# Kernel optimization log

Hardware: AMD Instinct MI355X
Metric: run time of the kernel (lower is better)

Reference implementation:

```python
import jax, jax.numpy as jnp
import numpy as np

NEG_SLOPE = 0.2
N_NODES, N_EDGES, N_FEAT, N_GRAPHS = 50000, 400000, 128, 64


def _glorot(k, shape):
    return jax.random.normal(k, shape, jnp.float32) / jnp.sqrt(jnp.float32(shape[0]))


def setup_inputs() -> dict:
    key = jax.random.key(0)
    ks = jax.random.split(key, 12)
    return {
        "x": jax.random.normal(ks[0], (N_NODES, N_FEAT), jnp.float32),
        "edge_index": jax.random.randint(ks[1], (2, N_EDGES), 0, N_NODES),
        "batch": jnp.sort(jax.random.randint(ks[2], (N_NODES,), 0, N_GRAPHS)),
        "W1": _glorot(ks[3], (N_FEAT, 64)),
        "as1": jax.random.normal(ks[4], (4, 16), jnp.float32) * 0.1,
        "ad1": jax.random.normal(ks[5], (4, 16), jnp.float32) * 0.1,
        "b1": jnp.zeros((64,), jnp.float32),
        "W2": _glorot(ks[6], (64, 256)),
        "as2": jax.random.normal(ks[7], (4, 64), jnp.float32) * 0.1,
        "ad2": jax.random.normal(ks[8], (4, 64), jnp.float32) * 0.1,
        "b2": jnp.zeros((256,), jnp.float32),
        "W3": _glorot(ks[9], (256, 512)),
        "as3": jax.random.normal(ks[10], (4, 128), jnp.float32) * 0.1,
        "ad3": jax.random.normal(ks[11], (4, 128), jnp.float32) * 0.1,
        "b3": jnp.zeros((128,), jnp.float32),
        "Wlin": _glorot(jax.random.fold_in(key, 99), (128, 10)),
        "blin": jnp.zeros((10,), jnp.float32),
    }


def _gat(x, src, dst, W, a_src, a_dst, b, concat, n):
    # PyG GATConv: per-head linear, LeakyReLU edge scores, segment softmax over
    # incoming edges of dst, weighted scatter-aggregate, then bias.
    H, C = a_src.shape
    h = (x @ W).reshape(n, H, C)                       # [N,H,C]
    es = jnp.einsum('nhc,hc->nh', h, a_src)            # score contrib of source node
    ed = jnp.einsum('nhc,hc->nh', h, a_dst)            # score contrib of target node
    e = jax.nn.leaky_relu(es[src] + ed[dst], NEG_SLOPE)  # [E,H]
    m = jax.ops.segment_max(e, dst, num_segments=n)
    m = jnp.where(jnp.isfinite(m), m, jnp.float32(0.0))
    ex = jnp.exp(e - m[dst])
    den = jax.ops.segment_sum(ex, dst, num_segments=n)
    alpha = ex / (den[dst] + jnp.float32(1e-16))       # [E,H]
    out = jax.ops.segment_sum(alpha[:, :, None] * h[src], dst, num_segments=n)  # [N,H,C]
    out = out.reshape(n, H * C) if concat else out.mean(axis=1)
    return out + b


def reference(x, edge_index, batch, W1, as1, ad1, b1, W2, as2, ad2, b2,
              W3, as3, ad3, b3, Wlin, blin):
    n = x.shape[0]
    loop = jnp.arange(n)
    src = jnp.concatenate([edge_index[0], loop])  # add self-loops (PyG default)
    dst = jnp.concatenate([edge_index[1], loop])
    h = jax.nn.elu(_gat(x, src, dst, W1, as1, ad1, b1, True, n))
    h = jax.nn.elu(_gat(h, src, dst, W2, as2, ad2, b2, True, n))
    h = jax.nn.elu(_gat(h, src, dst, W3, as3, ad3, b3, False, n))
    # global mean pool over graphs
    s = jax.ops.segment_sum(h, batch, num_segments=N_GRAPHS)
    cnt = jax.ops.segment_sum(jnp.ones((n,), h.dtype), batch, num_segments=N_GRAPHS)
    pooled = s / jnp.maximum(cnt, jnp.float32(1.0))[:, None]
    # dropout is identity in eval mode
    return pooled @ Wlin + blin
```

## Files before the change

kernel.cpp:

```cpp
#include <hip/hip_runtime.h>
#include <math.h>

#define NNODES 50000
#define NEDGES 400000
#define ETOT   (NEDGES + NNODES)
#define NGRAPHS 64

typedef _Float16 f16;
typedef _Float16 f16x4 __attribute__((ext_vector_type(4)));
typedef _Float16 f16x8 __attribute__((ext_vector_type(8)));
typedef float f32x4 __attribute__((ext_vector_type(4)));

__device__ __forceinline__ float lrelu(float x){ return x >= 0.f ? x : 0.2f*x; }
__device__ __forceinline__ float eluf(float x){ return x > 0.f ? x : expm1f(x); }

__global__ void k_one(int* __restrict__ deg){
  int i = blockIdx.x*256 + threadIdx.x;
  if (i < NNODES) deg[i] = 1;
}
__global__ void k_hist(const int* __restrict__ ei, int* __restrict__ deg){
  int e = blockIdx.x*blockDim.x + threadIdx.x;
  if (e < NEDGES) atomicAdd(&deg[ei[NEDGES + e]], 1);
}
__global__ void k_scan1(const int* __restrict__ deg, int* __restrict__ part, int n){
  __shared__ int buf[256];
  int i = blockIdx.x*256 + threadIdx.x;
  buf[threadIdx.x] = (i<n)? deg[i] : 0;
  __syncthreads();
  for (int s=128; s>0; s>>=1){ if (threadIdx.x < s) buf[threadIdx.x]+=buf[threadIdx.x+s]; __syncthreads(); }
  if (threadIdx.x==0) part[blockIdx.x]=buf[0];
}
__global__ void k_scan2(const int* __restrict__ part, int* __restrict__ bpre, int* __restrict__ row_off_last, int nb){
  __shared__ int buf[256];
  int t = threadIdx.x;
  int v = (t<nb)? part[t] : 0;
  buf[t]=v; __syncthreads();
  for (int s=1;s<256;s<<=1){ int a = (t>=s)? buf[t-s]:0; __syncthreads(); buf[t]+=a; __syncthreads(); }
  if (t<nb) bpre[t] = buf[t]-v;
  if (t==255) row_off_last[0] = buf[255];
}
__global__ void k_scan3(const int* __restrict__ deg, const int* __restrict__ bpre, int* __restrict__ row_off, int n){
  __shared__ int buf[256];
  int t = threadIdx.x;
  int i = blockIdx.x*256 + t;
  int v = (i<n)? deg[i]:0;
  buf[t]=v; __syncthreads();
  for (int s=1;s<256;s<<=1){ int a=(t>=s)?buf[t-s]:0; __syncthreads(); buf[t]+=a; __syncthreads(); }
  if (i<n) row_off[i] = bpre[blockIdx.x] + buf[t]-v;
}
__global__ void k_selfpos(const int* __restrict__ row_off, int* __restrict__ csr_src,
                          int* __restrict__ csr_dst, int* __restrict__ cursor){
  int n = blockIdx.x*256 + threadIdx.x;
  if (n < NNODES){
    int p = row_off[n];
    csr_src[p] = n; csr_dst[p] = n;
    cursor[n] = 1;
  }
}
__global__ void k_scatter(const int* __restrict__ ei, const int* __restrict__ row_off,
                          int* __restrict__ cursor, int* __restrict__ csr_src, int* __restrict__ csr_dst){
  int e = blockIdx.x*blockDim.x + threadIdx.x;
  if (e < NEDGES){
    int s = ei[e], d = ei[NEDGES+e];
    int pos = row_off[d] + atomicAdd(&cursor[d],1);
    csr_src[pos] = s; csr_dst[pos] = d;
  }
}

__global__ void k_prep(const float* __restrict__ W1, const float* __restrict__ W2, const float* __restrict__ W3,
                       const float* __restrict__ as1, const float* __restrict__ ad1,
                       const float* __restrict__ as2, const float* __restrict__ ad2,
                       const float* __restrict__ as3, const float* __restrict__ ad3,
                       f16* __restrict__ BT1, f16* __restrict__ BT2, f16* __restrict__ BT3y,
                       f16* __restrict__ PT1, f16* __restrict__ PT2, f16* __restrict__ PT3){
  int u = blockIdx.x*256 + threadIdx.x;
  if (u < 8192){ int j=u>>7, k=u&127; BT1[j*128+k] = (f16)W1[(size_t)k*64+j]; return; }
  u -= 8192;
  if (u < 16384){ int col=u>>6, k=u&63; BT2[col*64+k] = (f16)W2[(size_t)k*256+col]; return; }
  u -= 16384;
  if (u < 131072){ int j=u>>8, k=u&255;
                   BT3y[(size_t)j*256+k] = (f16)W3[(size_t)k*512 + j]; return; }
  u -= 131072;
  if (u < 1024){
    int o=u>>6, k=u&63; float v=0.f;
    if (o<8){ int h=o&3; if ((k>>4)==h) v = ((o<4)?as1:ad1)[h*16 + (k&15)]; }
    PT1[u] = (f16)v; return; }
  u -= 1024;
  if (u < 1024){
    int o=u>>6, k=u&63; float v=0.f;
    if (o<8){ int h=o&3;
      const float* a=((o<4)?as2:ad2)+h*64; const float* w=W2+(size_t)k*256+h*64;
      for(int c=0;c<64;c++) v=fmaf(w[c],a[c],v); }
    PT2[u] = (f16)v; return; }
  u -= 1024;
  if (u < 4096){
    int o=u>>8, k=u&255; float v=0.f;
    if (o<8){ int h=o&3;
      const float* a=((o<4)?as3:ad3)+h*128; const float* w=W3+(size_t)k*512+h*128;
      for(int c=0;c<128;c++) v=fmaf(w[c],a[c],v); }
    PT3[u] = (f16)v; }
}

__global__ void k_cvt_x(const float* __restrict__ x, f16* __restrict__ xh){
  int u = blockIdx.x*256 + threadIdx.x;
  if (u < NNODES*32){
    float4 v = *(const float4*)&x[(size_t)u*4];
    f16x4 o; o[0]=(f16)v.x; o[1]=(f16)v.y; o[2]=(f16)v.z; o[3]=(f16)v.w;
    *(f16x4*)&xh[(size_t)u*4] = o;
  }
}

template<int KF>
__global__ __launch_bounds__(256) void k_scores_m(const f16* __restrict__ g, const f16* __restrict__ PT,
                                                  float* __restrict__ esd){
  int wv = threadIdx.x>>6, lane = threadIdx.x&63;
  int r = lane&15, kb = lane>>4;
  int row0 = blockIdx.x*64 + wv*16;
  const f16* arow = g + (size_t)(row0+r)*KF + kb*8;
  const f16* brow = PT + (size_t)r*KF + kb*8;
  f32x4 acc = {0,0,0,0};
  #pragma unroll
  for (int k0=0;k0<KF;k0+=32){
    f16x8 af = *(const f16x8*)(arow + k0);
    f16x8 bf = *(const f16x8*)(brow + k0);
    acc = __builtin_amdgcn_mfma_f32_16x16x32_f16(af, bf, acc, 0,0,0);
  }
  if (r < 8){
    #pragma unroll
    for (int i=0;i<4;i++){
      int row = row0 + kb*4 + i;
      if (row < NNODES) esd[(size_t)row*8 + r] = acc[i];
    }
  }
}

__global__ __launch_bounds__(256) void k_expw(const float* __restrict__ esd, const int* __restrict__ csr_src,
                                              const int* __restrict__ csr_dst, float* __restrict__ alphaW){
  int p = blockIdx.x*256 + threadIdx.x;
  if (p >= ETOT) return;
  int s = csr_src[p], d = csr_dst[p];
  float4 a = *(const float4*)&esd[(size_t)s*8];
  float4 b = *(const float4*)&esd[(size_t)d*8+4];
  float4 r;
  r.x = expf(lrelu(a.x+b.x));
  r.y = expf(lrelu(a.y+b.y));
  r.z = expf(lrelu(a.z+b.z));
  r.w = expf(lrelu(a.w+b.w));
  *(float4*)&alphaW[(size_t)p*4] = r;
}

__global__ __launch_bounds__(256) void k_mfma_l1(const f16* __restrict__ xh, const f16* __restrict__ BT1,
                                                 f16* __restrict__ h1h){
  int wv = threadIdx.x>>6, lane = threadIdx.x&63;
  int r = lane&15, kb = lane>>4;
  int row0 = blockIdx.x*64 + wv*16;
  const f16* arow = xh + (size_t)(row0 + r)*128 + kb*8;
  f32x4 acc[4] = {{0,0,0,0},{0,0,0,0},{0,0,0,0},{0,0,0,0}};
  for (int k0=0;k0<128;k0+=32){
    f16x8 af = *(const f16x8*)(arow + k0);
    #pragma unroll
    for (int c=0;c<4;c++){
      f16x8 bf = *(const f16x8*)(BT1 + (size_t)(c*16+r)*128 + k0 + kb*8);
      acc[c] = __builtin_amdgcn_mfma_f32_16x16x32_f16(af, bf, acc[c], 0,0,0);
    }
  }
  #pragma unroll
  for (int c=0;c<4;c++)
    #pragma unroll
    for (int i=0;i<4;i++){
      int row = row0 + kb*4 + i;
      if (row < NNODES) h1h[(size_t)row*64 + c*16 + r] = (f16)acc[c][i];
    }
}

__global__ __launch_bounds__(256) void k_mfma_l2(const f16* __restrict__ agg2h, const f16* __restrict__ BT2,
                                                 const float* __restrict__ b2, f16* __restrict__ g2h){
  int wv = threadIdx.x>>6, lane = threadIdx.x&63;
  int r = lane&15, kb = lane>>4;
  int h = blockIdx.y;
  int row0 = blockIdx.x*64 + wv*16;
  const f16* arow = agg2h + (size_t)(row0 + r)*256 + h*64 + kb*8;
  f32x4 acc[4] = {{0,0,0,0},{0,0,0,0},{0,0,0,0},{0,0,0,0}};
  #pragma unroll
  for (int k0=0;k0<64;k0+=32){
    f16x8 af = *(const f16x8*)(arow + k0);
    #pragma unroll
    for (int c=0;c<4;c++){
      f16x8 bf = *(const f16x8*)(BT2 + (size_t)(h*64+c*16+r)*64 + k0 + kb*8);
      acc[c] = __builtin_amdgcn_mfma_f32_16x16x32_f16(af, bf, acc[c], 0,0,0);
    }
  }
  #pragma unroll
  for (int c=0;c<4;c++){
    int col = h*64 + c*16 + r;
    float bb = b2[col];
    #pragma unroll
    for (int i=0;i<4;i++){
      int row = row0 + kb*4 + i;
      if (row < NNODES) g2h[(size_t)row*256 + col] = (f16)eluf(acc[c][i] + bb);
    }
  }
}

__global__ __launch_bounds__(256) void k_mfma_y3(const f16* __restrict__ g2h, const f16* __restrict__ BT3y,
                                                 f16* __restrict__ y3){
  int wv = threadIdx.x>>6, lane = threadIdx.x&63;
  int r = lane&15, kb = lane>>4;
  int row0 = blockIdx.x*128 + wv*32;
  int col0 = blockIdx.y*64;
  const f16* a0 = g2h + (size_t)(row0 + r)*256 + kb*8;
  const f16* a1 = a0 + (size_t)16*256;
  f32x4 acc[2][4];
  #pragma unroll
  for (int rt=0;rt<2;rt++)
    #pragma unroll
    for (int c=0;c<4;c++) acc[rt][c] = (f32x4){0,0,0,0};
  for (int k0=0;k0<256;k0+=32){
    f16x8 af0 = *(const f16x8*)(a0 + k0);
    f16x8 af1 = *(const f16x8*)(a1 + k0);
    #pragma unroll
    for (int c=0;c<4;c++){
      f16x8 bf = *(const f16x8*)(BT3y + (size_t)(col0+c*16+r)*256 + k0 + kb*8);
      acc[0][c] = __builtin_amdgcn_mfma_f32_16x16x32_f16(af0, bf, acc[0][c], 0,0,0);
      acc[1][c] = __builtin_amdgcn_mfma_f32_16x16x32_f16(af1, bf, acc[1][c], 0,0,0);
    }
  }
  #pragma unroll
  for (int rt=0;rt<2;rt++)
    #pragma unroll
    for (int c=0;c<4;c++){
      int col = col0 + c*16 + r;
      #pragma unroll
      for (int i=0;i<4;i++){
        int row = row0 + rt*16 + kb*4 + i;
        if (row < NNODES) y3[(size_t)row*512 + col] = (f16)acc[rt][c][i];
      }
    }
}

__global__ __launch_bounds__(256) void k_gat1f(const f16* __restrict__ h1h, const float* __restrict__ alphaW,
    const int* __restrict__ row_off, const int* __restrict__ csr_src,
    const float* __restrict__ b1, f16* __restrict__ g1h){
  int n = blockIdx.x*4 + (threadIdx.x>>6);
  if (n >= NNODES) return;
  int t = threadIdx.x & 63;
  int head = t >> 4;
  int pos = row_off[n], end = row_off[n+1];
  float acc = 0.f, den = 0.f;
  for (; pos+1 < end; pos += 2){
    int s0 = csr_src[pos], s1 = csr_src[pos+1];
    float w0 = alphaW[(size_t)pos*4 + head];
    float w1 = alphaW[(size_t)(pos+1)*4 + head];
    float v0 = (float)h1h[(size_t)s0*64 + t];
    float v1 = (float)h1h[(size_t)s1*64 + t];
    acc = fmaf(w0, v0, fmaf(w1, v1, acc));
    den += w0 + w1;
  }
  if (pos < end){
    int s0 = csr_src[pos];
    float w0 = alphaW[(size_t)pos*4 + head];
    acc = fmaf(w0, (float)h1h[(size_t)s0*64 + t], acc);
    den += w0;
  }
  g1h[(size_t)n*64 + t] = (f16)eluf(acc/(den + 1e-16f) + b1[t]);
}

__global__ __launch_bounds__(256) void k_agg2f(const f16* __restrict__ g1h, const float* __restrict__ alphaW,
    const int* __restrict__ row_off, const int* __restrict__ csr_src,
    f16* __restrict__ agg2h){
  int n = blockIdx.x*4 + (threadIdx.x>>6);
  if (n >= NNODES) return;
  int t = threadIdx.x & 63;
  int pos = row_off[n], end = row_off[n+1];
  float c0=0.f,c1=0.f,c2=0.f,c3=0.f,d0=0.f,d1=0.f,d2=0.f,d3=0.f;
  for (; pos+1 < end; pos += 2){
    int s0 = csr_src[pos], s1 = csr_src[pos+1];
    float4 a = *(const float4*)&alphaW[(size_t)pos*4];
    float4 b = *(const float4*)&alphaW[(size_t)(pos+1)*4];
    float v0 = (float)g1h[(size_t)s0*64 + t];
    float v1 = (float)g1h[(size_t)s1*64 + t];
    c0=fmaf(a.x,v0,fmaf(b.x,v1,c0)); c1=fmaf(a.y,v0,fmaf(b.y,v1,c1));
    c2=fmaf(a.z,v0,fmaf(b.z,v1,c2)); c3=fmaf(a.w,v0,fmaf(b.w,v1,c3));
    d0+=a.x+b.x; d1+=a.y+b.y; d2+=a.z+b.z; d3+=a.w+b.w;
  }
  if (pos < end){
    int s0 = csr_src[pos];
    float4 a = *(const float4*)&alphaW[(size_t)pos*4];
    float v0 = (float)g1h[(size_t)s0*64 + t];
    c0=fmaf(a.x,v0,c0); c1=fmaf(a.y,v0,c1); c2=fmaf(a.z,v0,c2); c3=fmaf(a.w,v0,c3);
    d0+=a.x; d1+=a.y; d2+=a.z; d3+=a.w;
  }
  size_t base = (size_t)n*256;
  agg2h[base       + t] = (f16)(c0/(d0+1e-16f));
  agg2h[base +  64 + t] = (f16)(c1/(d1+1e-16f));
  agg2h[base + 128 + t] = (f16)(c2/(d2+1e-16f));
  agg2h[base + 192 + t] = (f16)(c3/(d3+1e-16f));
}

__global__ __launch_bounds__(256) void k_agg3y(const f16* __restrict__ y3, const float* __restrict__ alphaW,
    const int* __restrict__ row_off, const int* __restrict__ csr_src,
    const float* __restrict__ b3, float* __restrict__ g3){
  int n = blockIdx.x*4 + (threadIdx.x>>6);
  if (n >= NNODES) return;
  int lane = threadIdx.x & 63;
  int head = lane >> 4;
  int coff = lane*8;
  int pos = row_off[n], end = row_off[n+1];
  float acc[8] = {};
  float den = 0.f;
  for (; pos+1 < end; pos += 2){
    int s0 = csr_src[pos], s1 = csr_src[pos+1];
    float w0 = alphaW[(size_t)pos*4 + head];
    float w1 = alphaW[(size_t)(pos+1)*4 + head];
    f16x8 u0 = *(const f16x8*)&y3[(size_t)s0*512 + coff];
    f16x8 u1 = *(const f16x8*)&y3[(size_t)s1*512 + coff];
    #pragma unroll
    for (int j=0;j<8;j++)
      acc[j] = fmaf(w0, (float)u0[j], fmaf(w1, (float)u1[j], acc[j]));
    den += w0 + w1;
  }
  if (pos < end){
    int s0 = csr_src[pos];
    float w0 = alphaW[(size_t)pos*4 + head];
    f16x8 u0 = *(const f16x8*)&y3[(size_t)s0*512 + coff];
    #pragma unroll
    for (int j=0;j<8;j++)
      acc[j] = fmaf(w0, (float)u0[j], acc[j]);
    den += w0;
  }
  float inv = 1.f/(den + 1e-16f);
  #pragma unroll
  for (int j=0;j<8;j++){
    float r = acc[j]*inv;
    r += __shfl_xor(r, 16, 64);
    r += __shfl_xor(r, 32, 64);
    acc[j] = r;
  }
  if (lane < 16){
    int c0 = lane*8;
    #pragma unroll
    for (int j=0;j<8;j++)
      g3[(size_t)n*128 + c0 + j] = eluf(0.25f*acc[j] + b3[c0+j]);
  }
}

__device__ __forceinline__ int lowerb(const int* a, int n, int v){
  int lo=0, hi=n;
  while (lo<hi){ int mid=(lo+hi)>>1; if (a[mid]<v) lo=mid+1; else hi=mid; }
  return lo;
}
__global__ void k_pool8(const float* __restrict__ g3, const int* __restrict__ batch, float* __restrict__ pooledS){
  int g = blockIdx.x, ch = blockIdx.y, c = threadIdx.x;
  int lo = lowerb(batch, NNODES, g);
  int hi = lowerb(batch, NNODES, g+1);
  int len = hi - lo;
  int b0 = lo + (len*ch)/8, b1 = lo + (len*(ch+1))/8;
  float s = 0.f;
  for (int nn=b0; nn<b1; ++nn) s += g3[(size_t)nn*128 + c];
  if (b1 > b0) atomicAdd(&pooledS[g*128+c], s);
}
__global__ void k_lin(const float* __restrict__ pooledS, const int* __restrict__ batch,
                      const float* __restrict__ Wlin, const float* __restrict__ blin, float* __restrict__ out){
  int t = threadIdx.x;
  if (t < 640){
    int g = t/10, j = t%10;
    int lo = lowerb(batch, NNODES, g);
    int hi = lowerb(batch, NNODES, g+1);
    float inv = 1.f / fmaxf((float)(hi-lo), 1.f);
    float s = blin[j];
    for (int c=0;c<128;c++) s = fmaf(pooledS[g*128+c]*inv, Wlin[c*10+j], s);
    out[t] = s;
  }
}

extern "C" void kernel_launch(void* const* d_in, const int* in_sizes, int n_in,
                              void* d_out, int out_size, void* d_ws, size_t ws_size,
                              hipStream_t stream){
  (void)in_sizes; (void)n_in; (void)out_size; (void)ws_size;
  const float* x    = (const float*)d_in[0];
  const int*   ei   = (const int*)d_in[1];
  const int*   batch= (const int*)d_in[2];
  const float* W1   = (const float*)d_in[3];
  const float* as1  = (const float*)d_in[4];
  const float* ad1  = (const float*)d_in[5];
  const float* b1   = (const float*)d_in[6];
  const float* W2   = (const float*)d_in[7];
  const float* as2  = (const float*)d_in[8];
  const float* ad2  = (const float*)d_in[9];
  const float* b2   = (const float*)d_in[10];
  const float* W3   = (const float*)d_in[11];
  const float* as3  = (const float*)d_in[12];
  const float* ad3  = (const float*)d_in[13];
  const float* b3   = (const float*)d_in[14];
  const float* Wlin = (const float*)d_in[15];
  const float* blin = (const float*)d_in[16];
  float* out = (float*)d_out;

  char* ws = (char*)d_ws;
  size_t off = 0;
  auto alloc = [&](size_t bytes)->char*{ char* p = ws + off; off += (bytes + 255) & ~(size_t)255; return p; };
  int* csr_src = (int*)alloc((size_t)ETOT*4);
  int* csr_dst = (int*)alloc((size_t)ETOT*4);
  int* row_off = (int*)alloc((size_t)(NNODES+1)*4);
  int* deg     = (int*)alloc((size_t)NNODES*4);
  int* cursor  = (int*)alloc((size_t)NNODES*4);
  int* part    = (int*)alloc(256*4);
  int* bpre    = (int*)alloc(256*4);
  float* esd   = (float*)alloc((size_t)NNODES*8*4);
  float* alphaW= (float*)alloc((size_t)ETOT*4*4);
  f16* BT1     = (f16*)alloc(8192*2);
  f16* BT2     = (f16*)alloc(16384*2);
  f16* BT3y    = (f16*)alloc(131072*2);
  f16* PT1     = (f16*)alloc(1024*2);
  f16* PT2     = (f16*)alloc(1024*2);
  f16* PT3     = (f16*)alloc(4096*2);
  float* pooledS = (float*)alloc((size_t)NGRAPHS*128*4);
  f16* xh      = (f16*)alloc((size_t)NNODES*128*2);
  f16* h1h     = (f16*)alloc((size_t)NNODES*64*2);
  f16* g1h     = (f16*)alloc((size_t)NNODES*64*2);
  f16* agg2h   = (f16*)alloc((size_t)NNODES*256*2);
  f16* g2h     = (f16*)alloc((size_t)NNODES*256*2);
  f16* y3      = (f16*)alloc((size_t)NNODES*512*2);
  float* g3    = (float*)alloc((size_t)NNODES*128*4);

  int nbE = (NEDGES+255)/256;
  int nbS = (NNODES+255)/256;
  int nbP = (ETOT+255)/256;
  int nb4 = (NNODES+3)/4;

  k_one<<<nbS,256,0,stream>>>(deg);
  k_hist<<<nbE,256,0,stream>>>(ei, deg);
  k_scan1<<<nbS,256,0,stream>>>(deg, part, NNODES);
  k_scan2<<<1,256,0,stream>>>(part, bpre, row_off+NNODES, nbS);
  k_scan3<<<nbS,256,0,stream>>>(deg, bpre, row_off, NNODES);
  k_selfpos<<<nbS,256,0,stream>>>(row_off, csr_src, csr_dst, cursor);
  k_scatter<<<nbE,256,0,stream>>>(ei, row_off, cursor, csr_src, csr_dst);

  k_prep<<<632,256,0,stream>>>(W1,W2,W3,as1,ad1,as2,ad2,as3,ad3,BT1,BT2,BT3y,PT1,PT2,PT3);
  k_cvt_x<<<6250,256,0,stream>>>(x, xh);

  k_mfma_l1<<<782,256,0,stream>>>(xh, BT1, h1h);
  k_scores_m<64><<<782,256,0,stream>>>(h1h, PT1, esd);
  k_expw<<<nbP,256,0,stream>>>(esd, csr_src, csr_dst, alphaW);
  k_gat1f<<<nb4,256,0,stream>>>(h1h, alphaW, row_off, csr_src, b1, g1h);

  k_scores_m<64><<<782,256,0,stream>>>(g1h, PT2, esd);
  k_expw<<<nbP,256,0,stream>>>(esd, csr_src, csr_dst, alphaW);
  k_agg2f<<<nb4,256,0,stream>>>(g1h, alphaW, row_off, csr_src, agg2h);
  k_mfma_l2<<<dim3(782,4),256,0,stream>>>(agg2h, BT2, b2, g2h);

  k_scores_m<256><<<782,256,0,stream>>>(g2h, PT3, esd);
  k_mfma_y3<<<dim3(391,8),256,0,stream>>>(g2h, BT3y, y3);
  k_expw<<<nbP,256,0,stream>>>(esd, csr_src, csr_dst, alphaW);
  k_agg3y<<<nb4,256,0,stream>>>(y3, alphaW, row_off, csr_src, b3, g3);

  hipMemsetAsync(pooledS, 0, (size_t)NGRAPHS*128*4, stream);
  k_pool8<<<dim3(NGRAPHS,8),128,0,stream>>>(g3, batch, pooledS);
  k_lin<<<1,1024,0,stream>>>(pooledS, batch, Wlin, blin, out);
}
```

Before: 420.9 us.

## Fuse layer-3 score projection into y3 MFMA kernel with register-resident A rows

The layer-3 attention score computation (previously a separate k_scores_m pass over g2h) is folded into the y3 GEMM kernel as an extra 16-column MFMA tile using PT3. The kernel now loads each wave's 32 rows of g2h into registers once and loops over all 32 column tiles, instead of launching 8 column blocks that each reread the A rows. This removes one full read of g2h and one launch. The cost is a grid that shrinks from 3128 to 391 blocks, which lowers parallelism, plus more registers per thread for the A fragments.

```diff
diff --git a/kernel.cpp b/kernel.cpp
--- a/kernel.cpp
+++ b/kernel.cpp
@@ -202,40 +202,57 @@
   }
 }
 
-__global__ __launch_bounds__(256) void k_mfma_y3(const f16* __restrict__ g2h, const f16* __restrict__ BT3y,
-                                                 f16* __restrict__ y3){
+__global__ __launch_bounds__(256) void k_mfma_y3r(const f16* __restrict__ g2h, const f16* __restrict__ BT3y,
+                                                  const f16* __restrict__ PT3,
+                                                  f16* __restrict__ y3, float* __restrict__ esd){
   int wv = threadIdx.x>>6, lane = threadIdx.x&63;
   int r = lane&15, kb = lane>>4;
   int row0 = blockIdx.x*128 + wv*32;
-  int col0 = blockIdx.y*64;
   const f16* a0 = g2h + (size_t)(row0 + r)*256 + kb*8;
   const f16* a1 = a0 + (size_t)16*256;
-  f32x4 acc[2][4];
-  #pragma unroll
-  for (int rt=0;rt<2;rt++)
-    #pragma unroll
-    for (int c=0;c<4;c++) acc[rt][c] = (f32x4){0,0,0,0};
-  for (int k0=0;k0<256;k0+=32){
-    f16x8 af0 = *(const f16x8*)(a0 + k0);
-    f16x8 af1 = *(const f16x8*)(a1 + k0);
-    #pragma unroll
-    for (int c=0;c<4;c++){
-      f16x8 bf = *(const f16x8*)(BT3y + (size_t)(col0+c*16+r)*256 + k0 + kb*8);
-      acc[0][c] = __builtin_amdgcn_mfma_f32_16x16x32_f16(af0, bf, acc[0][c], 0,0,0);
-      acc[1][c] = __builtin_amdgcn_mfma_f32_16x16x32_f16(af1, bf, acc[1][c], 0,0,0);
-    }
-  }
-  #pragma unroll
-  for (int rt=0;rt<2;rt++)
-    #pragma unroll
-    for (int c=0;c<4;c++){
-      int col = col0 + c*16 + r;
+  f16x8 a[2][8];
+  #pragma unroll
+  for (int kk=0;kk<8;kk++){
+    a[0][kk] = *(const f16x8*)(a0 + kk*32);
+    a[1][kk] = *(const f16x8*)(a1 + kk*32);
+  }
+  for (int ct=0; ct<32; ++ct){
+    const f16* brow = BT3y + (size_t)(ct*16+r)*256 + kb*8;
+    f32x4 acc0 = {0,0,0,0}, acc1 = {0,0,0,0};
+    #pragma unroll
+    for (int kk=0;kk<8;kk++){
+      f16x8 bf = *(const f16x8*)(brow + kk*32);
+      acc0 = __builtin_amdgcn_mfma_f32_16x16x32_f16(a[0][kk], bf, acc0, 0,0,0);
+      acc1 = __builtin_amdgcn_mfma_f32_16x16x32_f16(a[1][kk], bf, acc1, 0,0,0);
+    }
+    int col = ct*16 + r;
+    #pragma unroll
+    for (int i=0;i<4;i++){
+      int row = row0 + kb*4 + i;
+      if (row < NNODES) y3[(size_t)row*512 + col] = (f16)acc0[i];
+      row += 16;
+      if (row < NNODES) y3[(size_t)row*512 + col] = (f16)acc1[i];
+    }
+  }
+  {
+    const f16* brow = PT3 + (size_t)r*256 + kb*8;
+    f32x4 acc0 = {0,0,0,0}, acc1 = {0,0,0,0};
+    #pragma unroll
+    for (int kk=0;kk<8;kk++){
+      f16x8 bf = *(const f16x8*)(brow + kk*32);
+      acc0 = __builtin_amdgcn_mfma_f32_16x16x32_f16(a[0][kk], bf, acc0, 0,0,0);
+      acc1 = __builtin_amdgcn_mfma_f32_16x16x32_f16(a[1][kk], bf, acc1, 0,0,0);
+    }
+    if (r < 8){
       #pragma unroll
       for (int i=0;i<4;i++){
-        int row = row0 + rt*16 + kb*4 + i;
-        if (row < NNODES) y3[(size_t)row*512 + col] = (f16)acc[rt][c][i];
+        int row = row0 + kb*4 + i;
+        if (row < NNODES) esd[(size_t)row*8 + r] = acc0[i];
+        row += 16;
+        if (row < NNODES) esd[(size_t)row*8 + r] = acc1[i];
       }
     }
+  }
 }
 
 __global__ __launch_bounds__(256) void k_gat1f(const f16* __restrict__ h1h, const float* __restrict__ alphaW,
@@ -449,8 +466,7 @@
   k_agg2f<<<nb4,256,0,stream>>>(g1h, alphaW, row_off, csr_src, agg2h);
   k_mfma_l2<<<dim3(782,4),256,0,stream>>>(agg2h, BT2, b2, g2h);
 
-  k_scores_m<256><<<782,256,0,stream>>>(g2h, PT3, esd);
-  k_mfma_y3<<<dim3(391,8),256,0,stream>>>(g2h, BT3y, y3);
+  k_mfma_y3r<<<391,256,0,stream>>>(g2h, BT3y, PT3, y3, esd);
   k_expw<<<nbP,256,0,stream>>>(esd, csr_src, csr_dst, alphaW);
   k_agg3y<<<nb4,256,0,stream>>>(y3, alphaW, row_off, csr_src, b3, g3);
 
```

Result: faster. 408.8 us (-2.9%).
